# Kernel tuning notes

Measured on AMD Instinct MI355X. Metric: run time of the kernel, lower is better.

## Reference

```python
import jax, jax.numpy as jnp
import numpy as np
import math

N, M_KV = 8192, 8192
QDIM, KDIM, MID = 256, 256, 128
NEG_BIG = -float(1 << 32)  # matches torch.masked_fill(Attn, mask, -(1 << 32))


def setup_inputs() -> dict:
    key = jax.random.key(0)
    ks = jax.random.split(key, 8)
    main_feat = jax.random.normal(ks[0], (N, QDIM), dtype=jnp.float32)
    other_feat = jax.random.normal(ks[1], (M_KV, KDIM), dtype=jnp.float32)
    fix_feat = jax.random.uniform(ks[2], (M_KV,), dtype=jnp.float32)
    mask = jax.random.randint(ks[3], (N, M_KV), 0, 2).astype(jnp.bool_)
    # Linear params (torch.nn.Linear stores weight as [out, in])
    Wq = jax.random.normal(ks[4], (MID, QDIM), dtype=jnp.float32) / math.sqrt(QDIM)
    bq = jax.random.normal(ks[5], (MID,), dtype=jnp.float32) * 0.01
    Wk = jax.random.normal(ks[6], (MID, KDIM), dtype=jnp.float32) / math.sqrt(KDIM)
    bk = jax.random.normal(ks[7], (MID,), dtype=jnp.float32) * 0.01
    return {"main_feat": main_feat, "other_feat": other_feat, "fix_feat": fix_feat,
            "mask": mask, "Wq": Wq, "bq": bq, "Wk": Wk, "bk": bk}


def reference(main_feat, other_feat, fix_feat, mask, Wq, bq, Wk, bk):
    # Projections: y = x @ W.T + b
    Q = main_feat @ Wq.T + bq            # [N, MID]
    K = other_feat @ Wk.T + bk           # [M, MID]
    scale = 1.0 / math.sqrt(MID)
    attn = jnp.einsum('nd,md->nm', Q, K) * scale   # [N, M]
    attn = jnp.where(mask, NEG_BIG, attn)
    attn = jax.nn.softmax(attn, axis=-1)
    # diag(fix_feat) @ other_feat is just a row-wise scale of V
    V = fix_feat[:, None] * other_feat   # [M, KDIM]
    return attn @ V                      # [N, KDIM]
```

## Files before the change

kernel.cpp:

```cpp
#include <hip/hip_runtime.h>
#include <hip/hip_bf16.h>
#include <stdint.h>

typedef __attribute__((ext_vector_type(8))) short short8;
typedef __attribute__((ext_vector_type(4))) float floatx4;

#define MFMA32K(a, b, c) __builtin_amdgcn_mfma_f32_16x16x32_bf16(a, b, c, 0, 0, 0)

constexpr int N_Q  = 8192;
constexpr int M_KV = 8192;
constexpr int DMID = 128;
constexpr int DV   = 256;

__device__ __forceinline__ unsigned short f2bf(float x) {
    unsigned u = __float_as_uint(x);
    u += 0x7fffu + ((u >> 16) & 1u);
    return (unsigned short)(u >> 16);
}

__device__ __forceinline__ short8 cvt_f8_bf8(float4 a, float4 b) {
    short8 r;
    r[0] = (short)f2bf(a.x); r[1] = (short)f2bf(a.y);
    r[2] = (short)f2bf(a.z); r[3] = (short)f2bf(a.w);
    r[4] = (short)f2bf(b.x); r[5] = (short)f2bf(b.y);
    r[6] = (short)f2bf(b.z); r[7] = (short)f2bf(b.w);
    return r;
}

__device__ __forceinline__ void gl_lds16(const unsigned short* g, unsigned short* l) {
    __builtin_amdgcn_global_load_lds(
        (const __attribute__((address_space(1))) unsigned int*)g,
        (__attribute__((address_space(3))) unsigned int*)l, 16, 0, 0);
}

__device__ __forceinline__ unsigned nz4(unsigned x) {
    unsigned nz = (((x & 0x7f7f7f7fu) + 0x7f7f7f7fu) | x) & 0x80808080u;
    unsigned a = (nz >> 7) & 0x01010101u;
    return (a * 0x01020408u) >> 24;
}

__global__ __launch_bounds__(256) void proj_kernel(
    const float* __restrict__ main_feat, const float* __restrict__ Wq, const float* __restrict__ bq,
    const float* __restrict__ other_feat, const float* __restrict__ Wk, const float* __restrict__ bk,
    unsigned short* __restrict__ Qw, unsigned short* __restrict__ Kw)
{
    const float* src;  const float* W;  const float* bias;  unsigned short* dst;
    if (blockIdx.y == 0) { src = main_feat;  W = Wq; bias = bq; dst = Qw; }
    else                 { src = other_feat; W = Wk; bias = bk; dst = Kw; }

    const int wave = threadIdx.x >> 6, lane = threadIdx.x & 63;
    const int n = lane & 15, quad = lane >> 4;
    const int row0 = blockIdx.x * 64 + wave * 16;

    short8 a[8];
    const float* ap = src + (size_t)(row0 + n) * 256 + quad * 8;
#pragma unroll
    for (int ks = 0; ks < 8; ++ks) {
        float4 x0 = *(const float4*)(ap + ks * 32);
        float4 x1 = *(const float4*)(ap + ks * 32 + 4);
        a[ks] = cvt_f8_bf8(x0, x1);
    }

    floatx4 acc[8];
#pragma unroll
    for (int nt = 0; nt < 8; ++nt) acc[nt] = floatx4{0.f, 0.f, 0.f, 0.f};

#pragma unroll
    for (int nt = 0; nt < 8; ++nt) {
        const float* wp = W + (size_t)(nt * 16 + n) * 256 + quad * 8;
#pragma unroll
        for (int ks = 0; ks < 8; ++ks) {
            float4 w0 = *(const float4*)(wp + ks * 32);
            float4 w1 = *(const float4*)(wp + ks * 32 + 4);
            short8 b = cvt_f8_bf8(w0, w1);
            acc[nt] = MFMA32K(a[ks], b, acc[nt]);
        }
    }

#pragma unroll
    for (int nt = 0; nt < 8; ++nt) {
        float bb = bias[nt * 16 + n];
#pragma unroll
        for (int reg = 0; reg < 4; ++reg) {
            int r = row0 + quad * 4 + reg;
            int c = nt * 16 + n;
            int phys = ((((c >> 3) + r) & 15) << 3) | (c & 7);
            dst[(size_t)r * DMID + phys] = f2bf(acc[nt][reg] + bb);
        }
    }
}

__global__ __launch_bounds__(256) void build_vt_kernel(
    const float* __restrict__ other_feat, const float* __restrict__ fix_feat,
    unsigned short* __restrict__ Vt)
{
    __shared__ unsigned short tile[64 * 72];
    const int t = threadIdx.x;
    const int m0 = blockIdx.x * 64, d0 = blockIdx.y * 64;

#pragma unroll
    for (int r = 0; r < 4; ++r) {
        int idx = r * 256 + t;
        int ml = idx >> 4, dl4 = (idx & 15) * 4;
        float4 v = *(const float4*)(other_feat + (size_t)(m0 + ml) * 256 + d0 + dl4);
        float f = fix_feat[m0 + ml];
        tile[(dl4 + 0) * 72 + ml] = f2bf(v.x * f);
        tile[(dl4 + 1) * 72 + ml] = f2bf(v.y * f);
        tile[(dl4 + 2) * 72 + ml] = f2bf(v.z * f);
        tile[(dl4 + 3) * 72 + ml] = f2bf(v.w * f);
    }
    __syncthreads();
#pragma unroll
    for (int r = 0; r < 8; ++r) {
        int dl = r * 8 + (t >> 5);
        int d = d0 + dl;
        int ml = (t & 31) * 2;
        int e = ml >> 5, s = (ml >> 4) & 1, q = (ml >> 2) & 3, j = ml & 3;
        int pc = e * 32 + q * 8 + s * 4 + j;
        int phys = ((((pc >> 3) + d) & 7) << 3) | (pc & 7);
        unsigned int v0 = tile[dl * 72 + ml];
        unsigned int v1 = tile[dl * 72 + ml + 1];
        *(unsigned int*)(Vt + (size_t)d * M_KV + m0 + phys) = v0 | (v1 << 16);
    }
}

template<int ESZ>
__device__ __forceinline__ void flash_body(
    const unsigned short* __restrict__ Qw, const unsigned short* __restrict__ Kw,
    const unsigned short* __restrict__ Vt, const unsigned int* __restrict__ mask,
    unsigned short* __restrict__ Opart, float* __restrict__ Lpart,
    int nsplit, int lgNs,
    unsigned short* k_lds , unsigned short* vt_lds )
{
    const int L = blockIdx.x + gridDim.x * blockIdx.y;
    const int ly = L & (nsplit - 1);
    const int lx = L >> lgNs;
    const int chunkLen = M_KV >> lgNs;
    const int mBeg = ly * chunkLen;
    const int tid = threadIdx.x;
    const int wave = tid >> 6, lane = tid & 63, n = lane & 15, quad = lane >> 4;
    const int qrow0 = lx * 128 + wave * 32;
    constexpr float SC = 0.08838834764831845f * 1.4426950408889634f;

    short8 qf[2][4];
#pragma unroll
    for (int qt = 0; qt < 2; ++qt)
#pragma unroll
        for (int db = 0; db < 4; ++db) {
            int row = qrow0 + qt * 16 + n;
            int phys = (db * 4 + quad + row) & 15;
            qf[qt][db] = *(const short8*)(Qw + (size_t)row * DMID + phys * 8);
        }

    floatx4 Oacc[2][16];
#pragma unroll
    for (int qt = 0; qt < 2; ++qt)
#pragma unroll
        for (int dt = 0; dt < 16; ++dt) Oacc[qt][dt] = floatx4{0.f, 0.f, 0.f, 0.f};

    float lrow[2] = {0.f, 0.f};

    const unsigned short* kg = Kw + (size_t)(wave * 4 + (lane >> 4)) * DMID + (lane & 15) * 8;
    const unsigned short* vg = Vt + (size_t)(wave * 8 + (lane >> 3)) * M_KV + (lane & 7) * 8;
    unsigned short* vld = &vt_lds[wave * 512];
    const int kqn = quad + n;

    uint4    mv4[2][4];
    unsigned mv1[2][4];

    auto load_mask = [&](int m0l) {
#pragma unroll
        for (int qt = 0; qt < 2; ++qt) {
            const size_t row = (size_t)(qrow0 + qt * 16 + n);
            if constexpr (ESZ == 4) {
                const unsigned* mp = mask + row * M_KV + m0l + quad * 4;
#pragma unroll
                for (int kvt = 0; kvt < 4; ++kvt)
                    mv4[qt][kvt] = *(const uint4*)(mp + kvt * 16);
            } else {
                const unsigned* mp = mask + row * (M_KV / 4) + (m0l >> 2) + quad;
#pragma unroll
                for (int kvt = 0; kvt < 4; ++kvt)
                    mv1[qt][kvt] = mp[kvt * 4];
            }
        }
    };

#pragma unroll
    for (int r = 0; r < 4; ++r)
        gl_lds16(kg + (size_t)(mBeg + r * 16) * DMID, &k_lds[wave * 512 + r * 2048]);
    load_mask(mBeg);

    const int iters = chunkLen / 64;
    for (int it = 0; it < iters; ++it) {
        const int m0 = mBeg + it * 64;
        const unsigned short* kbuf = k_lds + (it & 1) * 8192;

        __syncthreads();

#pragma unroll
        for (int r = 0; r < 8; ++r)
            gl_lds16(vg + (size_t)(r * 32) * M_KV + m0, vld + r * 2048);

        unsigned wq[2];
#pragma unroll
        for (int qt = 0; qt < 2; ++qt) {
            unsigned b = 0;
            if constexpr (ESZ == 4) {
#pragma unroll
                for (int kvt = 0; kvt < 4; ++kvt) {
                    const unsigned* c = (const unsigned*)&mv4[qt][kvt];
#pragma unroll
                    for (int j = 0; j < 4; ++j)
                        b |= (c[j] != 0u ? 1u : 0u) << (kvt * 4 + j);
                }
            } else {
#pragma unroll
                for (int kvt = 0; kvt < 4; ++kvt)
                    b |= nz4(mv1[qt][kvt]) << (kvt * 4);
            }
            wq[qt] = b;
        }

        floatx4 ST[4][2];
        __builtin_amdgcn_s_setprio(1);
#pragma unroll
        for (int kvt = 0; kvt < 4; ++kvt) {
            const int rowoff = (kvt * 16 + n) * DMID;
            short8 a0 = *(const short8*)&kbuf[rowoff + (((kqn + 0) & 15) << 3)];
            short8 a1 = *(const short8*)&kbuf[rowoff + (((kqn + 4) & 15) << 3)];
            short8 a2 = *(const short8*)&kbuf[rowoff + (((kqn + 8) & 15) << 3)];
            short8 a3 = *(const short8*)&kbuf[rowoff + (((kqn + 12) & 15) << 3)];
#pragma unroll
            for (int qt = 0; qt < 2; ++qt) {
                floatx4 s = floatx4{0.f, 0.f, 0.f, 0.f};
                s = MFMA32K(a0, qf[qt][0], s);
                s = MFMA32K(a1, qf[qt][1], s);
                s = MFMA32K(a2, qf[qt][2], s);
                s = MFMA32K(a3, qf[qt][3], s);
                ST[kvt][qt] = s;
            }
        }
        __builtin_amdgcn_s_setprio(0);

        short8 pf8[2][2];
#pragma unroll
        for (int qt = 0; qt < 2; ++qt) {
            const unsigned x = wq[qt];
            float lacc = 0.f;
#pragma unroll
            for (int kvt = 0; kvt < 4; ++kvt) {
                int e = kvt >> 1, s = kvt & 1;
                float p[4];
#pragma unroll
                for (int j = 0; j < 4; ++j) {
                    float v = __builtin_amdgcn_exp2f(ST[kvt][qt][j] * SC);
                    p[j] = ((x >> (kvt * 4 + j)) & 1u) ? 0.f : v;
                    lacc += p[j];
                }
                __hip_bfloat162 h0 = __float22bfloat162_rn(make_float2(p[0], p[1]));
                __hip_bfloat162 h1 = __float22bfloat162_rn(make_float2(p[2], p[3]));
                unsigned u0, u1;
                __builtin_memcpy(&u0, &h0, 4);
                __builtin_memcpy(&u1, &h1, 4);
                ((unsigned*)&pf8[qt][e])[s * 2 + 0] = u0;
                ((unsigned*)&pf8[qt][e])[s * 2 + 1] = u1;
            }
            lrow[qt] += lacc;
        }

        __syncthreads();

        if (it + 1 < iters) {
            unsigned short* knext = k_lds + ((it + 1) & 1) * 8192 + wave * 512;
#pragma unroll
            for (int r = 0; r < 4; ++r)
                gl_lds16(kg + (size_t)(m0 + 64 + r * 16) * DMID, knext + r * 2048);
            load_mask(m0 + 64);
        }

        __builtin_amdgcn_s_setprio(1);
#pragma unroll
        for (int e = 0; e < 2; ++e) {
#pragma unroll
            for (int dt = 0; dt < 16; ++dt) {
                const int vb = (dt * 16 + n) * 64 + (((e * 4 + quad + n) & 7) << 3);
                short8 bv = *(const short8*)&vt_lds[vb];
                Oacc[0][dt] = MFMA32K(pf8[0][e], bv, Oacc[0][dt]);
                Oacc[1][dt] = MFMA32K(pf8[1][e], bv, Oacc[1][dt]);
            }
        }
        __builtin_amdgcn_s_setprio(0);
    }

    const size_t obase = (size_t)ly * N_Q * DV;
#pragma unroll
    for (int qt = 0; qt < 2; ++qt)
#pragma unroll
        for (int dt = 0; dt < 16; ++dt)
#pragma unroll
            for (int reg = 0; reg < 4; ++reg) {
                int gr = qrow0 + qt * 16 + quad * 4 + reg;
                Opart[obase + (size_t)gr * DV + dt * 16 + n] = f2bf(Oacc[qt][dt][reg]);
            }
#pragma unroll
    for (int qt = 0; qt < 2; ++qt) {
        float r = lrow[qt];
        r += __shfl_xor(r, 16);
        r += __shfl_xor(r, 32);
        if (quad == 0)
            Lpart[ly * N_Q + qrow0 + qt * 16 + n] = r;
    }
}

__global__ __launch_bounds__(256, 2) void flash_kernel(
    const unsigned short* __restrict__ Qw, const unsigned short* __restrict__ Kw,
    const unsigned short* __restrict__ Vt, const unsigned int* __restrict__ mask,
    unsigned short* __restrict__ Opart, float* __restrict__ Lpart,
    int nsplit, int lgNs)
{
    __shared__ __align__(16) unsigned short k_lds[2][64 * 128];
    __shared__ __align__(16) unsigned short vt_lds[256 * 64];

    unsigned w0 = mask[threadIdx.x & 63];
    bool isf = (w0 == 0x3f800000u);
    bool isb = (w0 > 1u) && !isf;
    bool wide = (__ballot(isf) != 0ull) || (__ballot(isb) == 0ull);

    if (wide)
        flash_body<4>(Qw, Kw, Vt, mask, Opart, Lpart, nsplit, lgNs,
                      &k_lds[0][0], vt_lds);
    else
        flash_body<1>(Qw, Kw, Vt, mask, Opart, Lpart, nsplit, lgNs,
                      &k_lds[0][0], vt_lds);
}

__global__ __launch_bounds__(256) void combine_kernel(
    const unsigned short* __restrict__ Opart, const float* __restrict__ Lpart,
    float* __restrict__ out, int nsplit)
{
    const int row = blockIdx.x, d = threadIdx.x;
    float L = 0.f, o = 0.f;
    for (int c = 0; c < nsplit; ++c) {
        L += Lpart[c * N_Q + row];
        unsigned int b = Opart[((size_t)c * N_Q + row) * DV + d];
        o += __uint_as_float(b << 16);
    }
    out[(size_t)row * DV + d] = o / L;
}

extern "C" void kernel_launch(void* const* d_in, const int* in_sizes, int n_in,
                              void* d_out, int out_size, void* d_ws, size_t ws_size,
                              hipStream_t stream)
{
    const float* main_feat  = (const float*)d_in[0];
    const float* other_feat = (const float*)d_in[1];
    const float* fix_feat   = (const float*)d_in[2];
    const void*  mask       = d_in[3];
    const float* Wq         = (const float*)d_in[4];
    const float* bq         = (const float*)d_in[5];
    const float* Wk         = (const float*)d_in[6];
    const float* bk         = (const float*)d_in[7];
    float* out = (float*)d_out;

    char* ws = (char*)d_ws;
    unsigned short* Qw = (unsigned short*)(ws);
    unsigned short* Kw = (unsigned short*)(ws + (1ull << 21));
    unsigned short* Vt = (unsigned short*)(ws + (2ull << 21));
    float* Lpart = (float*)(ws + (16ull << 20) + 2048);

    const size_t base = (16ull << 20) + 2048;
    auto need = [&](int ns) {
        return base + (size_t)ns * N_Q * 4 + (size_t)ns * N_Q * DV * 2;
    };
    int nsplit = 1, lgNs = 0;
    if (ws_size >= need(8))      { nsplit = 8; lgNs = 3; }
    else if (ws_size >= need(4)) { nsplit = 4; lgNs = 2; }
    else if (ws_size >= need(2)) { nsplit = 2; lgNs = 1; }

    unsigned short* Opart = (unsigned short*)(Lpart + (size_t)nsplit * N_Q);

    hipLaunchKernelGGL(proj_kernel, dim3(128, 2), dim3(256), 0, stream,
                       main_feat, Wq, bq, other_feat, Wk, bk, Qw, Kw);
    hipLaunchKernelGGL(build_vt_kernel, dim3(128, 4), dim3(256), 0, stream,
                       other_feat, fix_feat, Vt);
    hipLaunchKernelGGL(flash_kernel, dim3(64, nsplit), dim3(256), 0, stream,
                       Qw, Kw, Vt, (const unsigned int*)mask, Opart, Lpart, nsplit, lgNs);
    hipLaunchKernelGGL(combine_kernel, dim3(N_Q), dim3(256), 0, stream,
                       Opart, Lpart, out, nsplit);
}
```

Baseline: 471.8 us.

## Replace global_load_lds with register-staged prefetch pipeline for K and Vt tiles

Direct global-to-LDS loads for the K and transposed V tiles are replaced with loads into registers that are later written to LDS, with K prefetched two iterations ahead and Vt one iteration ahead. The barriers become explicit lgkmcnt waits plus s_barrier, so they no longer wait on outstanding global (vmcnt) loads. The goal is to hide global memory latency behind the QK and PV MFMA work. In exchange it adds about 48 VGPRs of staging registers, which may lower occupancy or cause spills, and it adds VALU/LDS store instructions.

```diff
diff --git a/kernel.cpp b/kernel.cpp
--- a/kernel.cpp
+++ b/kernel.cpp
@@ -27,10 +27,8 @@
     return r;
 }
 
-__device__ __forceinline__ void gl_lds16(const unsigned short* g, unsigned short* l) {
-    __builtin_amdgcn_global_load_lds(
-        (const __attribute__((address_space(1))) unsigned int*)g,
-        (__attribute__((address_space(3))) unsigned int*)l, 16, 0, 0);
+__device__ __forceinline__ void lgkm_barrier() {
+    asm volatile("s_waitcnt lgkmcnt(0)\n\ts_barrier" ::: "memory");
 }
 
 __device__ __forceinline__ unsigned nz4(unsigned x) {
@@ -162,12 +160,24 @@
 
     const unsigned short* kg = Kw + (size_t)(wave * 4 + (lane >> 4)) * DMID + (lane & 15) * 8;
     const unsigned short* vg = Vt + (size_t)(wave * 8 + (lane >> 3)) * M_KV + (lane & 7) * 8;
-    unsigned short* vld = &vt_lds[wave * 512];
+    const int kw_idx = wave * 512 + lane * 8;
+    const int vw_idx = wave * 512 + lane * 8;
     const int kqn = quad + n;
 
+    uint4 kreg[4], vreg[8];
     uint4    mv4[2][4];
     unsigned mv1[2][4];
 
+    auto load_K = [&](int m0l) {
+#pragma unroll
+        for (int r = 0; r < 4; ++r)
+            kreg[r] = *(const uint4*)(kg + (size_t)(m0l + r * 16) * DMID);
+    };
+    auto load_Vt = [&](int m0l) {
+#pragma unroll
+        for (int r = 0; r < 8; ++r)
+            vreg[r] = *(const uint4*)(vg + (size_t)(r * 32) * M_KV + m0l);
+    };
     auto load_mask = [&](int m0l) {
 #pragma unroll
         for (int qt = 0; qt < 2; ++qt) {
@@ -185,22 +195,32 @@
             }
         }
     };
-
-#pragma unroll
-    for (int r = 0; r < 4; ++r)
-        gl_lds16(kg + (size_t)(mBeg + r * 16) * DMID, &k_lds[wave * 512 + r * 2048]);
+    auto store_K = [&](int buf) {
+#pragma unroll
+        for (int r = 0; r < 4; ++r)
+            *(uint4*)&k_lds[buf * 8192 + kw_idx + r * 2048] = kreg[r];
+    };
+    auto store_Vt = [&]() {
+#pragma unroll
+        for (int r = 0; r < 8; ++r)
+            *(uint4*)&vt_lds[vw_idx + r * 2048] = vreg[r];
+    };
+
+    const int iters = chunkLen / 64;
+
+    load_K(mBeg);
+    store_K(0);
+    if (iters > 1) load_K(mBeg + 64);
+    load_Vt(mBeg);
     load_mask(mBeg);
 
-    const int iters = chunkLen / 64;
     for (int it = 0; it < iters; ++it) {
         const int m0 = mBeg + it * 64;
         const unsigned short* kbuf = k_lds + (it & 1) * 8192;
 
-        __syncthreads();
-
-#pragma unroll
-        for (int r = 0; r < 8; ++r)
-            gl_lds16(vg + (size_t)(r * 32) * M_KV + m0, vld + r * 2048);
+        lgkm_barrier();
+
+        store_Vt();
 
         unsigned wq[2];
 #pragma unroll
@@ -221,6 +241,13 @@
             }
             wq[qt] = b;
         }
+
+        if (it + 1 < iters) {
+            load_Vt(m0 + 64);
+            load_mask(m0 + 64);
+            store_K((it + 1) & 1);
+        }
+        if (it + 2 < iters) load_K(m0 + 128);
 
         floatx4 ST[4][2];
         __builtin_amdgcn_s_setprio(1);
@@ -269,15 +296,7 @@
             lrow[qt] += lacc;
         }
 
-        __syncthreads();
-
-        if (it + 1 < iters) {
-            unsigned short* knext = k_lds + ((it + 1) & 1) * 8192 + wave * 512;
-#pragma unroll
-            for (int r = 0; r < 4; ++r)
-                gl_lds16(kg + (size_t)(m0 + 64 + r * 16) * DMID, knext + r * 2048);
-            load_mask(m0 + 64);
-        }
+        lgkm_barrier();
 
         __builtin_amdgcn_s_setprio(1);
 #pragma unroll
```

Measured after the change: 651.9 us. 38.2% more time.

## Load mask cooperatively with coalesced rows and share compressed bitmap via LDS

Applied to the files above, without the earlier changes.

Replaces the per-wave strided mask loads, where each lane fetched small scattered pieces of its own rows, with a block-cooperative scheme. Threads read contiguous 64-byte or 256-byte row segments, compress them to bitmaps, and write those into a double-buffered LDS bitmap that each wave then reads and reshuffles into its MFMA lane layout. The goal is more coalesced global traffic for the large mask stream and fewer registers holding raw mask data. In exchange it adds LDS writes and reads plus bit-extraction ALU work each iteration, and the byte-mask path leaves half the threads idle during loading.

```diff
diff --git a/kernel.cpp b/kernel.cpp
--- a/kernel.cpp
+++ b/kernel.cpp
@@ -130,7 +130,8 @@
     const unsigned short* __restrict__ Vt, const unsigned int* __restrict__ mask,
     unsigned short* __restrict__ Opart, float* __restrict__ Lpart,
     int nsplit, int lgNs,
-    unsigned short* k_lds , unsigned short* vt_lds )
+    unsigned short* k_lds , unsigned short* vt_lds ,
+    unsigned long long* bm )
 {
     const int L = blockIdx.x + gridDim.x * blockIdx.y;
     const int ly = L & (nsplit - 1);
@@ -139,7 +140,8 @@
     const int mBeg = ly * chunkLen;
     const int tid = threadIdx.x;
     const int wave = tid >> 6, lane = tid & 63, n = lane & 15, quad = lane >> 4;
-    const int qrow0 = lx * 128 + wave * 32;
+    const int qblk0 = lx * 128;
+    const int qrow0 = qblk0 + wave * 32;
     constexpr float SC = 0.08838834764831845f * 1.4426950408889634f;
 
     short8 qf[2][4];
@@ -165,36 +167,73 @@
     unsigned short* vld = &vt_lds[wave * 512];
     const int kqn = quad + n;
 
-    uint4    mv4[2][4];
-    unsigned mv1[2][4];
-
-    auto load_mask = [&](int m0l) {
+    const int lr4  = tid >> 2;
+    const int c16q = tid & 3;
+    uint4 vA[4], vB[4];
+
+    auto issue_raw = [&](int m0l, int r2, uint4* v) {
+        if constexpr (ESZ == 4) {
+            const uint4* p = (const uint4*)(mask + (size_t)(qblk0 + r2 * 64 + lr4) * M_KV
+                                            + m0l + c16q * 16);
+#pragma unroll
+            for (int k = 0; k < 4; ++k) v[k] = p[k];
+        } else {
+            if (tid < 128) {
+                const uint4* p = (const uint4*)((const unsigned char*)mask
+                                 + (size_t)(qblk0 + tid) * M_KV + m0l);
+#pragma unroll
+                for (int k = 0; k < 4; ++k) v[k] = p[k];
+            }
+        }
+    };
+    auto compress_write = [&](int buf, int r2, const uint4* v) {
+        if constexpr (ESZ == 4) {
+            unsigned b = 0;
+#pragma unroll
+            for (int k = 0; k < 4; ++k) {
+                b |= (v[k].x != 0u ? 1u : 0u) << (k * 4 + 0);
+                b |= (v[k].y != 0u ? 1u : 0u) << (k * 4 + 1);
+                b |= (v[k].z != 0u ? 1u : 0u) << (k * 4 + 2);
+                b |= (v[k].w != 0u ? 1u : 0u) << (k * 4 + 3);
+            }
+            *(unsigned short*)((char*)bm + buf * 1024 + (r2 * 64 + lr4) * 8 + c16q * 2)
+                = (unsigned short)b;
+        } else {
+            if (tid < 128) {
+                unsigned lo = nz4(v[0].x) | (nz4(v[0].y) << 4) | (nz4(v[0].z) << 8) | (nz4(v[0].w) << 12)
+                            | (nz4(v[1].x) << 16) | (nz4(v[1].y) << 20) | (nz4(v[1].z) << 24) | (nz4(v[1].w) << 28);
+                unsigned hi = nz4(v[2].x) | (nz4(v[2].y) << 4) | (nz4(v[2].z) << 8) | (nz4(v[2].w) << 12)
+                            | (nz4(v[3].x) << 16) | (nz4(v[3].y) << 20) | (nz4(v[3].z) << 24) | (nz4(v[3].w) << 28);
+                bm[buf * 128 + tid] = ((unsigned long long)hi << 32) | lo;
+            }
+        }
+    };
+    unsigned wq[2];
+    auto read_wq = [&](int buf) {
+        const unsigned q4 = quad * 4;
 #pragma unroll
         for (int qt = 0; qt < 2; ++qt) {
-            const size_t row = (size_t)(qrow0 + qt * 16 + n);
-            if constexpr (ESZ == 4) {
-                const unsigned* mp = mask + row * M_KV + m0l + quad * 4;
-#pragma unroll
-                for (int kvt = 0; kvt < 4; ++kvt)
-                    mv4[qt][kvt] = *(const uint4*)(mp + kvt * 16);
-            } else {
-                const unsigned* mp = mask + row * (M_KV / 4) + (m0l >> 2) + quad;
-#pragma unroll
-                for (int kvt = 0; kvt < 4; ++kvt)
-                    mv1[qt][kvt] = mp[kvt * 4];
-            }
+            int lr = wave * 32 + qt * 16 + n;
+            uint2 w = *(const uint2*)((const char*)bm + buf * 1024 + lr * 8);
+            wq[qt] = ((w.x >> q4) & 0xFu) | (((w.x >> (16 + q4)) & 0xFu) << 4)
+                   | (((w.y >> q4) & 0xFu) << 8) | (((w.y >> (16 + q4)) & 0xFu) << 12);
         }
     };
+
+    const int iters = chunkLen / 64;
 
 #pragma unroll
     for (int r = 0; r < 4; ++r)
         gl_lds16(kg + (size_t)(mBeg + r * 16) * DMID, &k_lds[wave * 512 + r * 2048]);
-    load_mask(mBeg);
-
-    const int iters = chunkLen / 64;
+    issue_raw(mBeg, 0, vA);
+    if constexpr (ESZ == 4) issue_raw(mBeg, 1, vB);
+    compress_write(0, 0, vA);
+    if constexpr (ESZ == 4) compress_write(0, 1, vB);
+
     for (int it = 0; it < iters; ++it) {
         const int m0 = mBeg + it * 64;
         const unsigned short* kbuf = k_lds + (it & 1) * 8192;
+        const int buf = it & 1, nbuf = buf ^ 1;
 
         __syncthreads();
 
@@ -202,25 +241,7 @@
         for (int r = 0; r < 8; ++r)
             gl_lds16(vg + (size_t)(r * 32) * M_KV + m0, vld + r * 2048);
 
-        unsigned wq[2];
-#pragma unroll
-        for (int qt = 0; qt < 2; ++qt) {
-            unsigned b = 0;
-            if constexpr (ESZ == 4) {
-#pragma unroll
-                for (int kvt = 0; kvt < 4; ++kvt) {
-                    const unsigned* c = (const unsigned*)&mv4[qt][kvt];
-#pragma unroll
-                    for (int j = 0; j < 4; ++j)
-                        b |= (c[j] != 0u ? 1u : 0u) << (kvt * 4 + j);
-                }
-            } else {
-#pragma unroll
-                for (int kvt = 0; kvt < 4; ++kvt)
-                    b |= nz4(mv1[qt][kvt]) << (kvt * 4);
-            }
-            wq[qt] = b;
-        }
+        read_wq(buf);
 
         floatx4 ST[4][2];
         __builtin_amdgcn_s_setprio(1);
@@ -276,7 +297,8 @@
 #pragma unroll
             for (int r = 0; r < 4; ++r)
                 gl_lds16(kg + (size_t)(m0 + 64 + r * 16) * DMID, knext + r * 2048);
-            load_mask(m0 + 64);
+            issue_raw(m0 + 64, 0, vA);
+            if constexpr (ESZ == 4) issue_raw(m0 + 64, 1, vB);
         }
 
         __builtin_amdgcn_s_setprio(1);
@@ -291,6 +313,11 @@
             }
         }
         __builtin_amdgcn_s_setprio(0);
+
+        if (it + 1 < iters) {
+            compress_write(nbuf, 0, vA);
+            if constexpr (ESZ == 4) compress_write(nbuf, 1, vB);
+        }
     }
 
     const size_t obase = (size_t)ly * N_Q * DV;
@@ -321,6 +348,7 @@
 {
     __shared__ __align__(16) unsigned short k_lds[2][64 * 128];
     __shared__ __align__(16) unsigned short vt_lds[256 * 64];
+    __shared__ __align__(16) unsigned long long bitmap[2][128];
 
     unsigned w0 = mask[threadIdx.x & 63];
     bool isf = (w0 == 0x3f800000u);
@@ -329,10 +357,10 @@
 
     if (wide)
         flash_body<4>(Qw, Kw, Vt, mask, Opart, Lpart, nsplit, lgNs,
-                      &k_lds[0][0], vt_lds);
+                      &k_lds[0][0], vt_lds, &bitmap[0][0]);
     else
         flash_body<1>(Qw, Kw, Vt, mask, Opart, Lpart, nsplit, lgNs,
-                      &k_lds[0][0], vt_lds);
+                      &k_lds[0][0], vt_lds, &bitmap[0][0]);
 }
 
 __global__ __launch_bounds__(256) void combine_kernel(
```

New measurement: 489.8 us. +3.8%, slower.
